# Kernel tuning notes

Hardware: AMD Instinct MI355X
Metric: run time of the kernel (lower is better)

The kernel has to match this reference:

```python
import jax, jax.numpy as jnp
import numpy as np

B, S, D = 2, 2048, 1024
N_HEADS = 16
HEAD_DIM = D // N_HEADS  # 64, even for RoPE
THETA = 10000.0


def rope_tables(seq, head_dim, dtype=jnp.float32):
    half = head_dim // 2
    freqs = 1.0 / (THETA ** (jnp.arange(half, dtype=jnp.float32) / half))
    angles = jnp.arange(seq, dtype=jnp.float32)[:, None] * freqs[None, :]  # [S, half]
    return jnp.cos(angles).astype(dtype), jnp.sin(angles).astype(dtype)


def apply_rope_interleaved(x, cos, sin):
    # x: [b, h, s, d]; even/odd interleaving
    x_even = x[..., 0::2]
    x_odd = x[..., 1::2]
    r_even = x_even * cos - x_odd * sin
    r_odd = x_even * sin + x_odd * cos
    # interleave back: stack on last axis then reshape
    out = jnp.stack([r_even, r_odd], axis=-1).reshape(x.shape)
    return out


def setup_inputs() -> dict:
    key = jax.random.key(0)
    ks = jax.random.split(key, 6)
    scale = 1.0 / np.sqrt(D)
    return {
        "x": jax.random.normal(ks[0], (B, S, D), dtype=jnp.float32),
        "Wq": jax.random.normal(ks[1], (D, D), dtype=jnp.float32) * scale,
        "Wk": jax.random.normal(ks[2], (D, D), dtype=jnp.float32) * scale,
        "Wv": jax.random.normal(ks[3], (D, D), dtype=jnp.float32) * scale,
        "Wo": jax.random.normal(ks[4], (D, D), dtype=jnp.float32) * scale,
        "bo": jnp.zeros((D,), dtype=jnp.float32),
    }


def reference(x, Wq, Wk, Wv, Wo, bo):
    b, s, _ = x.shape
    # QKV projections (no bias), split heads -> [b, h, s, hd]
    def proj(W):
        return jnp.einsum('bsd,de->bse', x, W).reshape(b, s, N_HEADS, HEAD_DIM).transpose(0, 2, 1, 3)
    q, k, v = proj(Wq), proj(Wk), proj(Wv)

    cos, sin = rope_tables(s, HEAD_DIM, x.dtype)  # [s, hd//2]
    q = apply_rope_interleaved(q, cos, sin)
    k = apply_rope_interleaved(k, cos, sin)

    scale = 1.0 / jnp.sqrt(jnp.asarray(HEAD_DIM, dtype=x.dtype))
    scores = jnp.einsum('bhqd,bhkd->bhqk', q, k) * scale  # [b, h, s, s]
    causal = jnp.tril(jnp.ones((s, s), dtype=bool))
    scores = jnp.where(causal[None, None], scores, jnp.asarray(-jnp.inf, dtype=scores.dtype))
    attn = jax.nn.softmax(scores, axis=-1)
    ctx = jnp.einsum('bhqk,bhkd->bhqd', attn, v)  # [b, h, s, hd]
    ctx = ctx.transpose(0, 2, 1, 3).reshape(b, s, N_HEADS * HEAD_DIM)
    return jnp.einsum('bsd,de->bse', ctx, Wo) + bo
```

## Files before the change

### kernel.cpp

```cpp
#include <hip/hip_runtime.h>
#include <hip/hip_bf16.h>
#include <math.h>

constexpr int Bb   = 2;
constexpr int S    = 2048;
constexpr int D    = 1024;
constexpr int H    = 16;
constexpr int Dh   = 64;
constexpr int HALF = 32;
constexpr int M    = Bb * S;
constexpr int K    = 1024;
constexpr int N    = 1024;

typedef __attribute__((ext_vector_type(8))) short short8;
typedef __attribute__((ext_vector_type(4))) float f32x4;

__device__ __forceinline__ unsigned short f2bf(float f) {
    unsigned int u = __float_as_uint(f);
    unsigned int r = (u + 0x7fffu + ((u >> 16) & 1u)) >> 16;
    return (unsigned short)r;
}

__device__ __forceinline__ void gl_lds16(const unsigned short* g, unsigned short* lds_base) {
    __builtin_amdgcn_global_load_lds(
        (const __attribute__((address_space(1))) unsigned int*)g,
        (__attribute__((address_space(3))) unsigned int*)lds_base, 16, 0, 0);
}

__global__ __launch_bounds__(256) void prep_kernel(
    const float* __restrict__ x,
    const float* W0, const float* W1, const float* W2, const float* W3,
    unsigned short* __restrict__ xb,
    unsigned short* T0, unsigned short* T1, unsigned short* T2, unsigned short* T3,
    float* __restrict__ cosT, float* __restrict__ sinT)
{
    __shared__ float tile[64][65];
    const int bid = blockIdx.x;
    const int tid = threadIdx.x;

    if (bid < 256) {
        int idx = bid * 256 + tid;
        int s = idx >> 5;
        int i = idx & 31;
        double freq = exp(-(double)i * (log(10000.0) / 32.0));
        double ang  = (double)s * freq;
        cosT[idx] = (float)cos(ang);
        sinT[idx] = (float)sin(ang);
    } else if (bid < 256 + 4096) {
        size_t i = (size_t)(bid - 256) * 256 + tid;
        float4 v = *(const float4*)(x + i * 4);
        ushort4 pk;
        pk.x = f2bf(v.x); pk.y = f2bf(v.y); pk.z = f2bf(v.z); pk.w = f2bf(v.w);
        *(ushort4*)(xb + i * 4) = pk;
    } else {
        int wb = bid - 4352;
        int z  = wb >> 8;
        int rem = wb & 255;
        const float* W = (z == 0) ? W0 : (z == 1) ? W1 : (z == 2) ? W2 : W3;
        unsigned short* T = (z == 0) ? T0 : (z == 1) ? T1 : (z == 2) ? T2 : T3;
        const int bk = (rem >> 4) * 64;
        const int bn = (rem & 15) * 64;
        const int lr = tid >> 4;
        const int lc = (tid & 15) * 4;

        #pragma unroll
        for (int i = 0; i < 4; ++i) {
            int r = lr + i * 16;
            float4 v = *(const float4*)(W + (size_t)(bk + r) * N + bn + lc);
            tile[r][lc + 0] = v.x; tile[r][lc + 1] = v.y;
            tile[r][lc + 2] = v.z; tile[r][lc + 3] = v.w;
        }
        __syncthreads();
        #pragma unroll
        for (int i = 0; i < 4; ++i) {
            int nr = lr + i * 16;
            ushort4 pk;
            pk.x = f2bf(tile[lc + 0][nr]);
            pk.y = f2bf(tile[lc + 1][nr]);
            pk.z = f2bf(tile[lc + 2][nr]);
            pk.w = f2bf(tile[lc + 3][nr]);
            *(ushort4*)(T + (size_t)(bn + nr) * K + bk + lc) = pk;
        }
    }
}

__global__ __launch_bounds__(256) void gemm_qkv_kernel(
    const unsigned short* __restrict__ A,
    const unsigned short* __restrict__ BT,
    unsigned short* outQ, unsigned short* outK, unsigned short* outV,
    const float* __restrict__ cosT, const float* __restrict__ sinT)
{
    constexpr int AST = 128 * 32;
    constexpr int BST = 128 * 32;
    __shared__ __align__(16) unsigned short As[2 * AST];
    __shared__ __align__(16) unsigned short Bs[2 * BST];

    const int tid  = threadIdx.x;
    const int wave = tid >> 6;
    const int lane = tid & 63;
    const int col  = lane & 15;
    const int quad = lane >> 4;
    const int wy   = wave >> 1;
    const int wx   = wave & 1;

    const int mbase = blockIdx.y * 128;
    const int nbase = blockIdx.x * 128;

    const int srow   = lane >> 2;
    const int schunk = lane & 3;

    const unsigned short* pA0;
    const unsigned short* pA1;
    {
        int tr0 = wave * 16 + srow;
        int tr1 = 64 + wave * 16 + srow;
        pA0 = A + (size_t)(mbase + tr0) * K + ((schunk + (tr0 >> 1)) & 3) * 8;
        pA1 = A + (size_t)(mbase + tr1) * K + ((schunk + (tr1 >> 1)) & 3) * 8;
    }
    const unsigned short* pB0;
    const unsigned short* pB1;
    {
        int tr0 = wave * 16 + srow;
        int tr1 = 64 + wave * 16 + srow;
        pB0 = BT + (size_t)(nbase + tr0) * K + ((schunk + (tr0 >> 1)) & 3) * 8;
        pB1 = BT + (size_t)(nbase + tr1) * K + ((schunk + (tr1 >> 1)) & 3) * 8;
    }
    unsigned short* dA0 = &As[(wave * 16) * 32];
    unsigned short* dA1 = &As[(64 + wave * 16) * 32];
    unsigned short* dB0 = &Bs[(wave * 16) * 32];
    unsigned short* dB1 = &Bs[(64 + wave * 16) * 32];

    int aoff[4], boff[4];
    #pragma unroll
    for (int mi = 0; mi < 4; ++mi) {
        int r = wy * 64 + mi * 16 + col;
        aoff[mi] = r * 32 + ((quad - (r >> 1)) & 3) * 8;
    }
    #pragma unroll
    for (int ni = 0; ni < 4; ++ni) {
        int r = wx * 64 + ni * 16 + col;
        boff[ni] = r * 32 + ((quad - (r >> 1)) & 3) * 8;
    }

    f32x4 acc[4][4];
    #pragma unroll
    for (int mi = 0; mi < 4; ++mi)
        #pragma unroll
        for (int ni = 0; ni < 4; ++ni) acc[mi][ni] = (f32x4)0.f;

    auto stage = [&](int buf) {
        gl_lds16(pA0, dA0 + buf * AST);  pA0 += 32;
        gl_lds16(pA1, dA1 + buf * AST);  pA1 += 32;
        gl_lds16(pB0, dB0 + buf * BST);  pB0 += 32;
        gl_lds16(pB1, dB1 + buf * BST);  pB1 += 32;
    };
    auto compute = [&](int buf) {
        const unsigned short* Ac = &As[buf * AST];
        const unsigned short* Bc = &Bs[buf * BST];
        short8 af[4], bfr[4];
        #pragma unroll
        for (int mi = 0; mi < 4; ++mi) af[mi] = *(const short8*)&Ac[aoff[mi]];
        #pragma unroll
        for (int ni = 0; ni < 4; ++ni) bfr[ni] = *(const short8*)&Bc[boff[ni]];
        #pragma unroll
        for (int mi = 0; mi < 4; ++mi)
            #pragma unroll
            for (int ni = 0; ni < 4; ++ni)
                acc[mi][ni] = __builtin_amdgcn_mfma_f32_16x16x32_bf16(af[mi], bfr[ni], acc[mi][ni], 0, 0, 0);
    };

    stage(0);
    #pragma unroll 1
    for (int kk = 0; kk < 32; kk += 2) {
        __syncthreads();
        if (kk + 1 < 32) stage(1);
        compute(0);
        __syncthreads();
        if (kk + 2 < 32) stage(0);
        compute(1);
    }

    const int z = nbase >> 10;
    if (z < 2) {
        unsigned short* o = z ? outK : outQ;
        #pragma unroll
        for (int ni = 0; ni < 4; ++ni) {
            int nl = (nbase & 1023) + wx * 64 + ni * 16 + col;
            int h = nl >> 6, dh0 = nl & 63, p = dh0 >> 1;
            bool even = !(dh0 & 1);
            #pragma unroll
            for (int mi = 0; mi < 4; ++mi)
                #pragma unroll
                for (int reg = 0; reg < 4; ++reg) {
                    int m_g = mbase + wy * 64 + mi * 16 + quad * 4 + reg;
                    int b = m_g >> 11, s = m_g & 2047;
                    float v = acc[mi][ni][reg];
                    float part = __shfl_xor(v, 1, 64);
                    float c = cosT[s * HALF + p], sn = sinT[s * HALF + p];
                    float r = even ? (v * c - part * sn) : (v * c + part * sn);
                    o[((size_t)(b * H + h) * S + s) * Dh + dh0] = f2bf(r);
                }
        }
    } else {
        unsigned short* o = outV;
        #pragma unroll
        for (int ni = 0; ni < 4; ++ni) {
            int nl = (nbase & 1023) + wx * 64 + ni * 16 + col;
            int h = nl >> 6, dh0 = nl & 63;
            #pragma unroll
            for (int mi = 0; mi < 4; ++mi) {
                int m0g = mbase + wy * 64 + mi * 16 + quad * 4;
                int b = m0g >> 11, s = m0g & 2047;
                ushort4 pk;
                pk.x = f2bf(acc[mi][ni][0]);
                pk.y = f2bf(acc[mi][ni][1]);
                pk.z = f2bf(acc[mi][ni][2]);
                pk.w = f2bf(acc[mi][ni][3]);
                *(ushort4*)&o[((size_t)(b * H + h) * Dh + dh0) * S + s] = pk;
            }
        }
    }
}

__global__ __launch_bounds__(256) void gemm_out_kernel(
    const unsigned short* __restrict__ A,
    const unsigned short* __restrict__ BT,
    float* __restrict__ outO, const float* __restrict__ bias)
{
    constexpr int BK   = 64;
    constexpr int ABUF = 128 * BK;
    constexpr int BBUF = 64 * BK;
    __shared__ __align__(16) unsigned short As[2 * ABUF];
    __shared__ __align__(16) unsigned short Bs[2 * BBUF];

    const int tid  = threadIdx.x;
    const int wave = tid >> 6;
    const int lane = tid & 63;
    const int col  = lane & 15;
    const int quad = lane >> 4;
    const int wy   = wave >> 1;
    const int wx   = wave & 1;

    const int mbase = blockIdx.y * 128;
    const int nbase = blockIdx.x * 64;

    const int srow8 = lane >> 3;
    const int sch8  = lane & 7;

    const unsigned short* pA[4];
    unsigned short* dA[4];
    #pragma unroll
    for (int w = 0; w < 4; ++w) {
        int base = wave * 32 + w * 8;
        int tr = base + srow8;
        pA[w] = A + (size_t)(mbase + tr) * K + ((sch8 + (tr >> 1)) & 7) * 8;
        dA[w] = &As[base * BK];
    }
    const unsigned short* pB[2];
    unsigned short* dB[2];
    #pragma unroll
    for (int w = 0; w < 2; ++w) {
        int base = wave * 16 + w * 8;
        int tr = base + srow8;
        pB[w] = BT + (size_t)(nbase + tr) * K + ((sch8 + (tr >> 1)) & 7) * 8;
        dB[w] = &Bs[base * BK];
    }

    int aoff[2][4], boff[2][2];
    #pragma unroll
    for (int ks = 0; ks < 2; ++ks) {
        #pragma unroll
        for (int mi = 0; mi < 4; ++mi) {
            int r = wy * 64 + mi * 16 + col;
            aoff[ks][mi] = r * BK + (((ks * 4 + quad) - (r >> 1)) & 7) * 8;
        }
        #pragma unroll
        for (int ni = 0; ni < 2; ++ni) {
            int r = wx * 32 + ni * 16 + col;
            boff[ks][ni] = r * BK + (((ks * 4 + quad) - (r >> 1)) & 7) * 8;
        }
    }

    f32x4 acc[4][2];
    #pragma unroll
    for (int mi = 0; mi < 4; ++mi)
        #pragma unroll
        for (int ni = 0; ni < 2; ++ni) acc[mi][ni] = (f32x4)0.f;

    auto stage = [&](int buf) {
        #pragma unroll
        for (int w = 0; w < 4; ++w) { gl_lds16(pA[w], dA[w] + buf * ABUF); pA[w] += BK; }
        #pragma unroll
        for (int w = 0; w < 2; ++w) { gl_lds16(pB[w], dB[w] + buf * BBUF); pB[w] += BK; }
    };
    auto compute = [&](int buf) {
        const unsigned short* Ac = &As[buf * ABUF];
        const unsigned short* Bc = &Bs[buf * BBUF];
        #pragma unroll
        for (int ks = 0; ks < 2; ++ks) {
            short8 af[4], bfr[2];
            #pragma unroll
            for (int mi = 0; mi < 4; ++mi) af[mi] = *(const short8*)&Ac[aoff[ks][mi]];
            #pragma unroll
            for (int ni = 0; ni < 2; ++ni) bfr[ni] = *(const short8*)&Bc[boff[ks][ni]];
            #pragma unroll
            for (int mi = 0; mi < 4; ++mi)
                #pragma unroll
                for (int ni = 0; ni < 2; ++ni)
                    acc[mi][ni] = __builtin_amdgcn_mfma_f32_16x16x32_bf16(af[mi], bfr[ni], acc[mi][ni], 0, 0, 0);
        }
    };

    stage(0);
    #pragma unroll 1
    for (int kk = 0; kk < 16; kk += 2) {
        __syncthreads();
        if (kk + 1 < 16) stage(1);
        compute(0);
        __syncthreads();
        if (kk + 2 < 16) stage(0);
        compute(1);
    }

    #pragma unroll
    for (int ni = 0; ni < 2; ++ni) {
        int n_g = nbase + wx * 32 + ni * 16 + col;
        float bv = bias[n_g];
        #pragma unroll
        for (int mi = 0; mi < 4; ++mi)
            #pragma unroll
            for (int reg = 0; reg < 4; ++reg) {
                int m_g = mbase + wy * 64 + mi * 16 + quad * 4 + reg;
                outO[(size_t)m_g * N + n_g] = acc[mi][ni][reg] + bv;
            }
    }
}

__global__ __launch_bounds__(256) void attn_mfma_kernel(
    const unsigned short* __restrict__ q, const unsigned short* __restrict__ k,
    const unsigned short* __restrict__ vt, unsigned short* __restrict__ ctx)
{
    constexpr int TSZ = 64 * 64;
    __shared__ __align__(16) unsigned short Ks[4 * TSZ];
    __shared__ __align__(16) unsigned short Vs[4 * TSZ];
    __shared__ __align__(16) unsigned short Ps[4][16 * 72];

    const int tid  = threadIdx.x;
    const int wave = tid >> 6;
    const int lane = tid & 63;
    const int col  = lane & 15;
    const int quad = lane >> 4;
    const int l8   = lane >> 3, cp = lane & 7;

    const int bh = blockIdx.y;
    const unsigned short* qb = q  + (size_t)bh * S * Dh;
    const unsigned short* kb = k  + (size_t)bh * S * Dh;
    const unsigned short* vb = vt + (size_t)bh * Dh * S;
    const int b = bh >> 4, h = bh & 15;

    unsigned short* dk0 = &Ks[(wave * 16 + 0) * 64];
    unsigned short* dk1 = &Ks[(wave * 16 + 8) * 64];
    unsigned short* dv0 = &Vs[(wave * 16 + 0) * 64];
    unsigned short* dv1 = &Vs[(wave * 16 + 8) * 64];

    int foff[2][4];
    #pragma unroll
    for (int ks = 0; ks < 2; ++ks)
        #pragma unroll
        for (int nt = 0; nt < 4; ++nt) {
            int r = nt * 16 + col;
            foff[ks][nt] = r * 64 + (((ks * 4 + quad) - r) & 7) * 8;
        }
    int poffW[4][4];
    #pragma unroll
    for (int nt = 0; nt < 4; ++nt)
        #pragma unroll
        for (int reg = 0; reg < 4; ++reg)
            poffW[nt][reg] = (quad * 4 + reg) * 72 + nt * 16 + col;
    const int poffR0 = col * 72 + quad * 8;

    for (int phase = 0; phase < 2; ++phase) {
        const int qt  = phase ? (31 - (int)blockIdx.x) : (int)blockIdx.x;
        const int wr0 = qt * 64 + wave * 16;

        const unsigned short *pk0, *pk1, *pv0, *pv1, *ok0, *ok1, *ov0, *ov1;
        {
            int r0 = wave * 16 + l8, r1 = r0 + 8;
            pk0 = kb + (size_t)r0 * Dh + ((cp + r0) & 7) * 8;
            pk1 = kb + (size_t)r1 * Dh + ((cp + r1) & 7) * 8;
            pv0 = vb + (size_t)r0 * S + ((cp + r0) & 7) * 8;
            pv1 = vb + (size_t)r1 * S + ((cp + r1) & 7) * 8;
            ok0 = pk0 + 64 * Dh; ok1 = pk1 + 64 * Dh;
            ov0 = pv0 + 64;      ov1 = pv1 + 64;
        }

        __syncthreads();
        gl_lds16(pk0, dk0); gl_lds16(pk1, dk1);
        gl_lds16(pv0, dv0); gl_lds16(pv1, dv1);
        if (qt >= 1) {
            gl_lds16(ok0, dk0 + TSZ); gl_lds16(ok1, dk1 + TSZ);
            gl_lds16(ov0, dv0 + TSZ); gl_lds16(ov1, dv1 + TSZ);
        }
        pk0 += 128 * Dh; pk1 += 128 * Dh; pv0 += 128; pv1 += 128;
        ok0 += 128 * Dh; ok1 += 128 * Dh; ov0 += 128; ov1 += 128;

        short8 qfrag[2];
        #pragma unroll
        for (int ks = 0; ks < 2; ++ks)
            qfrag[ks] = *(const short8*)(qb + (size_t)(wr0 + col) * Dh + ks * 32 + quad * 8);

        f32x4 O[4];
        float lacc[4];
        #pragma unroll
        for (int nt = 0; nt < 4; ++nt) O[nt] = (f32x4)0.f;
        #pragma unroll
        for (int r = 0; r < 4; ++r) lacc[r] = 0.f;

        auto subtile = [&](const unsigned short* Kc, const unsigned short* Vc, int t) {
            f32x4 sacc[4];
            #pragma unroll
            for (int nt = 0; nt < 4; ++nt) sacc[nt] = (f32x4)0.f;
            #pragma unroll
            for (int ks = 0; ks < 2; ++ks)
                #pragma unroll
                for (int nt = 0; nt < 4; ++nt) {
                    short8 kf = *(const short8*)&Kc[foff[ks][nt]];
                    sacc[nt] = __builtin_amdgcn_mfma_f32_16x16x32_bf16(qfrag[ks], kf, sacc[nt], 0, 0, 0);
                }
            float pb[4][4];
            #pragma unroll
            for (int nt = 0; nt < 4; ++nt) {
                int key_l = nt * 16 + col;
                #pragma unroll
                for (int reg = 0; reg < 4; ++reg) {
                    float e = __expf(fmaf(sacc[nt][reg], 0.125f, -8.0f));
                    if (t == qt && key_l > wave * 16 + quad * 4 + reg) e = 0.f;
                    pb[nt][reg] = e;
                }
            }
            #pragma unroll
            for (int reg = 0; reg < 4; ++reg)
                lacc[reg] += (pb[0][reg] + pb[1][reg]) + (pb[2][reg] + pb[3][reg]);
            #pragma unroll
            for (int nt = 0; nt < 4; ++nt)
                #pragma unroll
                for (int reg = 0; reg < 4; ++reg)
                    Ps[wave][poffW[nt][reg]] = f2bf(pb[nt][reg]);
            #pragma unroll
            for (int ks = 0; ks < 2; ++ks) {
                short8 pf = *(const short8*)&Ps[wave][poffR0 + ks * 32];
                #pragma unroll
                for (int nt = 0; nt < 4; ++nt) {
                    short8 vf = *(const short8*)&Vc[foff[ks][nt]];
                    O[nt] = __builtin_amdgcn_mfma_f32_16x16x32_bf16(pf, vf, O[nt], 0, 0, 0);
                }
            }
        };

        const int nint = (qt >> 1) + 1;
        for (int i = 0; i < nint; ++i) {
            __syncthreads();
            const int ta = 2 * i;
            if (ta + 2 <= qt) {
                const int nb = ((i + 1) & 1) * 2 * TSZ;
                gl_lds16(pk0, dk0 + nb); gl_lds16(pk1, dk1 + nb);
                gl_lds16(pv0, dv0 + nb); gl_lds16(pv1, dv1 + nb);
                if (ta + 3 <= qt) {
                    gl_lds16(ok0, dk0 + nb + TSZ); gl_lds16(ok1, dk1 + nb + TSZ);
                    gl_lds16(ov0, dv0 + nb + TSZ); gl_lds16(ov1, dv1 + nb + TSZ);
                }
                pk0 += 128 * Dh; pk1 += 128 * Dh; pv0 += 128; pv1 += 128;
                ok0 += 128 * Dh; ok1 += 128 * Dh; ov0 += 128; ov1 += 128;
            }
            const unsigned short* Kc = &Ks[(i & 1) * 2 * TSZ];
            const unsigned short* Vc = &Vs[(i & 1) * 2 * TSZ];
            subtile(Kc, Vc, ta);
            if (ta + 1 <= qt) subtile(Kc + TSZ, Vc + TSZ, ta + 1);
        }

        #pragma unroll
        for (int reg = 0; reg < 4; ++reg) {
            float s = lacc[reg];
            #pragma unroll
            for (int off = 1; off <= 8; off <<= 1)
                s += __shfl_xor(s, off, 64);
            lacc[reg] = s;
        }

        #pragma unroll
        for (int reg = 0; reg < 4; ++reg) {
            float inv = 1.0f / lacc[reg];
            int rg = wr0 + quad * 4 + reg;
            unsigned short* dst = ctx + ((size_t)b * S + rg) * 1024 + h * 64 + col;
            #pragma unroll
            for (int nt = 0; nt < 4; ++nt)
                dst[nt * 16] = f2bf(O[nt][reg] * inv);
        }
    }
}

extern "C" void kernel_launch(void* const* d_in, const int* in_sizes, int n_in,
                              void* d_out, int out_size, void* d_ws, size_t ws_size,
                              hipStream_t stream) {
    const float* x  = (const float*)d_in[0];
    const float* Wq = (const float*)d_in[1];
    const float* Wk = (const float*)d_in[2];
    const float* Wv = (const float*)d_in[3];
    const float* Wo = (const float*)d_in[4];
    const float* bo = (const float*)d_in[5];
    float* out = (float*)d_out;

    const size_t MK  = (size_t)M * K;
    const size_t NK  = (size_t)N * K;
    const size_t QKV = (size_t)Bb * H * S * Dh;

    unsigned short* xb   = (unsigned short*)d_ws;
    unsigned short* WqT  = xb  + MK;
    unsigned short* WkT  = WqT + NK;
    unsigned short* WvT  = WkT + NK;
    unsigned short* WoT  = WvT + NK;
    unsigned short* qbuf = WoT + NK;
    unsigned short* kbuf = qbuf + QKV;
    unsigned short* vtb  = kbuf + QKV;
    unsigned short* ctxb = vtb  + QKV;
    float* cosT = (float*)(ctxb + QKV);
    float* sinT = cosT + (size_t)S * HALF;

    prep_kernel<<<5376, 256, 0, stream>>>(x, Wq, Wk, Wv, Wo,
                                          xb, WqT, WkT, WvT, WoT, cosT, sinT);

    gemm_qkv_kernel<<<dim3(24, 32), 256, 0, stream>>>(
        xb, WqT, qbuf, kbuf, vtb, cosT, sinT);

    attn_mfma_kernel<<<dim3(16, Bb * H), 256, 0, stream>>>(qbuf, kbuf, vtb, ctxb);

    gemm_out_kernel<<<dim3(16, 32), 256, 0, stream>>>(ctxb, WoT, out, bo);
}
```

Measured before the change: 200.6 us.

## Share K/V tile loads across paired query tiles in attention; shrink out-GEMM tile

The attention kernel now processes both of its paired query tiles (small and large) in a single pass over the key/value sequence. Each K/V tile is loaded into LDS once and reused by both query tiles, where before there were two separate sequential passes. This halves K/V traffic and barrier count per block, at the cost of more registers for the duplicated accumulators. Separately, the output GEMM tile is reduced from 128x64 to 64x64 and the grid doubled, which gives more blocks for occupancy on the many CUs.

```diff
diff --git a/kernel.cpp b/kernel.cpp
--- a/kernel.cpp
+++ b/kernel.cpp
@@ -228,7 +228,7 @@
     float* __restrict__ outO, const float* __restrict__ bias)
 {
     constexpr int BK   = 64;
-    constexpr int ABUF = 128 * BK;
+    constexpr int ABUF = 64 * BK;
     constexpr int BBUF = 64 * BK;
     __shared__ __align__(16) unsigned short As[2 * ABUF];
     __shared__ __align__(16) unsigned short Bs[2 * BBUF];
@@ -241,37 +241,30 @@
     const int wy   = wave >> 1;
     const int wx   = wave & 1;
 
-    const int mbase = blockIdx.y * 128;
+    const int mbase = blockIdx.y * 64;
     const int nbase = blockIdx.x * 64;
 
     const int srow8 = lane >> 3;
     const int sch8  = lane & 7;
 
-    const unsigned short* pA[4];
-    unsigned short* dA[4];
-    #pragma unroll
-    for (int w = 0; w < 4; ++w) {
-        int base = wave * 32 + w * 8;
-        int tr = base + srow8;
-        pA[w] = A + (size_t)(mbase + tr) * K + ((sch8 + (tr >> 1)) & 7) * 8;
-        dA[w] = &As[base * BK];
-    }
-    const unsigned short* pB[2];
-    unsigned short* dB[2];
+    const unsigned short *pA[2], *pB[2];
+    unsigned short *dA[2], *dB[2];
     #pragma unroll
     for (int w = 0; w < 2; ++w) {
         int base = wave * 16 + w * 8;
         int tr = base + srow8;
+        pA[w] = A  + (size_t)(mbase + tr) * K + ((sch8 + (tr >> 1)) & 7) * 8;
         pB[w] = BT + (size_t)(nbase + tr) * K + ((sch8 + (tr >> 1)) & 7) * 8;
+        dA[w] = &As[base * BK];
         dB[w] = &Bs[base * BK];
     }
 
-    int aoff[2][4], boff[2][2];
+    int aoff[2][2], boff[2][2];
     #pragma unroll
     for (int ks = 0; ks < 2; ++ks) {
         #pragma unroll
-        for (int mi = 0; mi < 4; ++mi) {
-            int r = wy * 64 + mi * 16 + col;
+        for (int mi = 0; mi < 2; ++mi) {
+            int r = wy * 32 + mi * 16 + col;
             aoff[ks][mi] = r * BK + (((ks * 4 + quad) - (r >> 1)) & 7) * 8;
         }
         #pragma unroll
@@ -281,15 +274,15 @@
         }
     }
 
-    f32x4 acc[4][2];
-    #pragma unroll
-    for (int mi = 0; mi < 4; ++mi)
+    f32x4 acc[2][2];
+    #pragma unroll
+    for (int mi = 0; mi < 2; ++mi)
         #pragma unroll
         for (int ni = 0; ni < 2; ++ni) acc[mi][ni] = (f32x4)0.f;
 
     auto stage = [&](int buf) {
         #pragma unroll
-        for (int w = 0; w < 4; ++w) { gl_lds16(pA[w], dA[w] + buf * ABUF); pA[w] += BK; }
+        for (int w = 0; w < 2; ++w) { gl_lds16(pA[w], dA[w] + buf * ABUF); pA[w] += BK; }
         #pragma unroll
         for (int w = 0; w < 2; ++w) { gl_lds16(pB[w], dB[w] + buf * BBUF); pB[w] += BK; }
     };
@@ -298,13 +291,13 @@
         const unsigned short* Bc = &Bs[buf * BBUF];
         #pragma unroll
         for (int ks = 0; ks < 2; ++ks) {
-            short8 af[4], bfr[2];
-            #pragma unroll
-            for (int mi = 0; mi < 4; ++mi) af[mi] = *(const short8*)&Ac[aoff[ks][mi]];
+            short8 af[2], bfr[2];
+            #pragma unroll
+            for (int mi = 0; mi < 2; ++mi) af[mi] = *(const short8*)&Ac[aoff[ks][mi]];
             #pragma unroll
             for (int ni = 0; ni < 2; ++ni) bfr[ni] = *(const short8*)&Bc[boff[ks][ni]];
             #pragma unroll
-            for (int mi = 0; mi < 4; ++mi)
+            for (int mi = 0; mi < 2; ++mi)
                 #pragma unroll
                 for (int ni = 0; ni < 2; ++ni)
                     acc[mi][ni] = __builtin_amdgcn_mfma_f32_16x16x32_bf16(af[mi], bfr[ni], acc[mi][ni], 0, 0, 0);
@@ -327,10 +320,10 @@
         int n_g = nbase + wx * 32 + ni * 16 + col;
         float bv = bias[n_g];
         #pragma unroll
-        for (int mi = 0; mi < 4; ++mi)
+        for (int mi = 0; mi < 2; ++mi)
             #pragma unroll
             for (int reg = 0; reg < 4; ++reg) {
-                int m_g = mbase + wy * 64 + mi * 16 + quad * 4 + reg;
+                int m_g = mbase + wy * 32 + mi * 16 + quad * 4 + reg;
                 outO[(size_t)m_g * N + n_g] = acc[mi][ni][reg] + bv;
             }
     }
@@ -352,7 +345,10 @@
     const int quad = lane >> 4;
     const int l8   = lane >> 3, cp = lane & 7;
 
-    const int bh = blockIdx.y;
+    const int bh  = blockIdx.y;
+    const int x   = blockIdx.x;
+    const int qtb = 31 - x;
+    const int qts = x;
     const unsigned short* qb = q  + (size_t)bh * S * Dh;
     const unsigned short* kb = k  + (size_t)bh * S * Dh;
     const unsigned short* vb = vt + (size_t)bh * Dh * S;
@@ -379,68 +375,71 @@
             poffW[nt][reg] = (quad * 4 + reg) * 72 + nt * 16 + col;
     const int poffR0 = col * 72 + quad * 8;
 
-    for (int phase = 0; phase < 2; ++phase) {
-        const int qt  = phase ? (31 - (int)blockIdx.x) : (int)blockIdx.x;
-        const int wr0 = qt * 64 + wave * 16;
-
-        const unsigned short *pk0, *pk1, *pv0, *pv1, *ok0, *ok1, *ov0, *ov1;
-        {
-            int r0 = wave * 16 + l8, r1 = r0 + 8;
-            pk0 = kb + (size_t)r0 * Dh + ((cp + r0) & 7) * 8;
-            pk1 = kb + (size_t)r1 * Dh + ((cp + r1) & 7) * 8;
-            pv0 = vb + (size_t)r0 * S + ((cp + r0) & 7) * 8;
-            pv1 = vb + (size_t)r1 * S + ((cp + r1) & 7) * 8;
-            ok0 = pk0 + 64 * Dh; ok1 = pk1 + 64 * Dh;
-            ov0 = pv0 + 64;      ov1 = pv1 + 64;
-        }
-
-        __syncthreads();
-        gl_lds16(pk0, dk0); gl_lds16(pk1, dk1);
-        gl_lds16(pv0, dv0); gl_lds16(pv1, dv1);
-        if (qt >= 1) {
-            gl_lds16(ok0, dk0 + TSZ); gl_lds16(ok1, dk1 + TSZ);
-            gl_lds16(ov0, dv0 + TSZ); gl_lds16(ov1, dv1 + TSZ);
-        }
-        pk0 += 128 * Dh; pk1 += 128 * Dh; pv0 += 128; pv1 += 128;
-        ok0 += 128 * Dh; ok1 += 128 * Dh; ov0 += 128; ov1 += 128;
-
-        short8 qfrag[2];
+    const unsigned short *pk0, *pk1, *pv0, *pv1, *ok0, *ok1, *ov0, *ov1;
+    {
+        int r0 = wave * 16 + l8, r1 = r0 + 8;
+        pk0 = kb + (size_t)r0 * Dh + ((cp + r0) & 7) * 8;
+        pk1 = kb + (size_t)r1 * Dh + ((cp + r1) & 7) * 8;
+        pv0 = vb + (size_t)r0 * S + ((cp + r0) & 7) * 8;
+        pv1 = vb + (size_t)r1 * S + ((cp + r1) & 7) * 8;
+        ok0 = pk0 + 64 * Dh; ok1 = pk1 + 64 * Dh;
+        ov0 = pv0 + 64;      ov1 = pv1 + 64;
+    }
+
+    gl_lds16(pk0, dk0); gl_lds16(pk1, dk1);
+    gl_lds16(pv0, dv0); gl_lds16(pv1, dv1);
+    gl_lds16(ok0, dk0 + TSZ); gl_lds16(ok1, dk1 + TSZ);
+    gl_lds16(ov0, dv0 + TSZ); gl_lds16(ov1, dv1 + TSZ);
+    pk0 += 128 * Dh; pk1 += 128 * Dh; pv0 += 128; pv1 += 128;
+    ok0 += 128 * Dh; ok1 += 128 * Dh; ov0 += 128; ov1 += 128;
+
+    short8 qfrag[2][2];
+    f32x4 O[2][4];
+    float lacc[2][4];
+    int wr0[2];
+    #pragma unroll
+    for (int qi = 0; qi < 2; ++qi) {
+        wr0[qi] = (qi ? qts : qtb) * 64 + wave * 16;
         #pragma unroll
         for (int ks = 0; ks < 2; ++ks)
-            qfrag[ks] = *(const short8*)(qb + (size_t)(wr0 + col) * Dh + ks * 32 + quad * 8);
-
-        f32x4 O[4];
-        float lacc[4];
-        #pragma unroll
-        for (int nt = 0; nt < 4; ++nt) O[nt] = (f32x4)0.f;
-        #pragma unroll
-        for (int r = 0; r < 4; ++r) lacc[r] = 0.f;
-
-        auto subtile = [&](const unsigned short* Kc, const unsigned short* Vc, int t) {
-            f32x4 sacc[4];
-            #pragma unroll
-            for (int nt = 0; nt < 4; ++nt) sacc[nt] = (f32x4)0.f;
-            #pragma unroll
-            for (int ks = 0; ks < 2; ++ks)
-                #pragma unroll
-                for (int nt = 0; nt < 4; ++nt) {
-                    short8 kf = *(const short8*)&Kc[foff[ks][nt]];
-                    sacc[nt] = __builtin_amdgcn_mfma_f32_16x16x32_bf16(qfrag[ks], kf, sacc[nt], 0, 0, 0);
-                }
+            qfrag[qi][ks] = *(const short8*)(qb + (size_t)(wr0[qi] + col) * Dh + ks * 32 + quad * 8);
+        #pragma unroll
+        for (int nt = 0; nt < 4; ++nt) O[qi][nt] = (f32x4)0.f;
+        #pragma unroll
+        for (int r = 0; r < 4; ++r) lacc[qi][r] = 0.f;
+    }
+
+    auto subtile = [&](const unsigned short* Kc, const unsigned short* Vc,
+                       int t, bool both) {
+        f32x4 sacc[2][4];
+        #pragma unroll
+        for (int nt = 0; nt < 4; ++nt) { sacc[0][nt] = (f32x4)0.f; sacc[1][nt] = (f32x4)0.f; }
+        #pragma unroll
+        for (int ks = 0; ks < 2; ++ks)
+            #pragma unroll
+            for (int nt = 0; nt < 4; ++nt) {
+                short8 kf = *(const short8*)&Kc[foff[ks][nt]];
+                sacc[0][nt] = __builtin_amdgcn_mfma_f32_16x16x32_bf16(qfrag[0][ks], kf, sacc[0][nt], 0, 0, 0);
+                if (both)
+                    sacc[1][nt] = __builtin_amdgcn_mfma_f32_16x16x32_bf16(qfrag[1][ks], kf, sacc[1][nt], 0, 0, 0);
+            }
+        const int nqi = both ? 2 : 1;
+        for (int qi = 0; qi < nqi; ++qi) {
+            const int qt_i = qi ? qts : qtb;
             float pb[4][4];
             #pragma unroll
             for (int nt = 0; nt < 4; ++nt) {
                 int key_l = nt * 16 + col;
                 #pragma unroll
                 for (int reg = 0; reg < 4; ++reg) {
-                    float e = __expf(fmaf(sacc[nt][reg], 0.125f, -8.0f));
-                    if (t == qt && key_l > wave * 16 + quad * 4 + reg) e = 0.f;
+                    float e = __expf(fmaf(sacc[qi][nt][reg], 0.125f, -8.0f));
+                    if (t == qt_i && key_l > wave * 16 + quad * 4 + reg) e = 0.f;
                     pb[nt][reg] = e;
                 }
             }
             #pragma unroll
             for (int reg = 0; reg < 4; ++reg)
-                lacc[reg] += (pb[0][reg] + pb[1][reg]) + (pb[2][reg] + pb[3][reg]);
+                lacc[qi][reg] += (pb[0][reg] + pb[1][reg]) + (pb[2][reg] + pb[3][reg]);
             #pragma unroll
             for (int nt = 0; nt < 4; ++nt)
                 #pragma unroll
@@ -452,49 +451,48 @@
                 #pragma unroll
                 for (int nt = 0; nt < 4; ++nt) {
                     short8 vf = *(const short8*)&Vc[foff[ks][nt]];
-                    O[nt] = __builtin_amdgcn_mfma_f32_16x16x32_bf16(pf, vf, O[nt], 0, 0, 0);
+                    O[qi][nt] = __builtin_amdgcn_mfma_f32_16x16x32_bf16(pf, vf, O[qi][nt], 0, 0, 0);
                 }
             }
-        };
-
-        const int nint = (qt >> 1) + 1;
-        for (int i = 0; i < nint; ++i) {
-            __syncthreads();
-            const int ta = 2 * i;
-            if (ta + 2 <= qt) {
-                const int nb = ((i + 1) & 1) * 2 * TSZ;
-                gl_lds16(pk0, dk0 + nb); gl_lds16(pk1, dk1 + nb);
-                gl_lds16(pv0, dv0 + nb); gl_lds16(pv1, dv1 + nb);
-                if (ta + 3 <= qt) {
-                    gl_lds16(ok0, dk0 + nb + TSZ); gl_lds16(ok1, dk1 + nb + TSZ);
-                    gl_lds16(ov0, dv0 + nb + TSZ); gl_lds16(ov1, dv1 + nb + TSZ);
-                }
-                pk0 += 128 * Dh; pk1 += 128 * Dh; pv0 += 128; pv1 += 128;
-                ok0 += 128 * Dh; ok1 += 128 * Dh; ov0 += 128; ov1 += 128;
+        }
+    };
+
+    const int nint = (qtb + 2) >> 1;
+    for (int i = 0; i < nint; ++i) {
+        __syncthreads();
+        const int ta = 2 * i;
+        if (ta + 2 <= qtb) {
+            const int nb = ((i + 1) & 1) * 2 * TSZ;
+            gl_lds16(pk0, dk0 + nb); gl_lds16(pk1, dk1 + nb);
+            gl_lds16(pv0, dv0 + nb); gl_lds16(pv1, dv1 + nb);
+            if (ta + 3 <= qtb) {
+                gl_lds16(ok0, dk0 + nb + TSZ); gl_lds16(ok1, dk1 + nb + TSZ);
+                gl_lds16(ov0, dv0 + nb + TSZ); gl_lds16(ov1, dv1 + nb + TSZ);
             }
-            const unsigned short* Kc = &Ks[(i & 1) * 2 * TSZ];
-            const unsigned short* Vc = &Vs[(i & 1) * 2 * TSZ];
-            subtile(Kc, Vc, ta);
-            if (ta + 1 <= qt) subtile(Kc + TSZ, Vc + TSZ, ta + 1);
-        }
-
+            pk0 += 128 * Dh; pk1 += 128 * Dh; pv0 += 128; pv1 += 128;
+            ok0 += 128 * Dh; ok1 += 128 * Dh; ov0 += 128; ov1 += 128;
+        }
+        const unsigned short* Kc = &Ks[(i & 1) * 2 * TSZ];
+        const unsigned short* Vc = &Vs[(i & 1) * 2 * TSZ];
+        subtile(Kc, Vc, ta, ta <= qts);
+        if (ta + 1 <= qtb)
+            subtile(Kc + TSZ, Vc + TSZ, ta + 1, ta + 1 <= qts);
+    }
+
+    #pragma unroll
+    for (int qi = 0; qi < 2; ++qi) {
         #pragma unroll
         for (int reg = 0; reg < 4; ++reg) {
-            float s = lacc[reg];
+            float s = lacc[qi][reg];
             #pragma unroll
             for (int off = 1; off <= 8; off <<= 1)
                 s += __shfl_xor(s, off, 64);
-            lacc[reg] = s;
-        }
-
-        #pragma unroll
-        for (int reg = 0; reg < 4; ++reg) {
-            float inv = 1.0f / lacc[reg];
-            int rg = wr0 + quad * 4 + reg;
+            float inv = 1.0f / s;
+            int rg = wr0[qi] + quad * 4 + reg;
             unsigned short* dst = ctx + ((size_t)b * S + rg) * 1024 + h * 64 + col;
             #pragma unroll
             for (int nt = 0; nt < 4; ++nt)
-                dst[nt * 16] = f2bf(O[nt][reg] * inv);
+                dst[nt * 16] = f2bf(O[qi][nt][reg] * inv);
         }
     }
 }
@@ -534,5 +532,5 @@
 
     attn_mfma_kernel<<<dim3(16, Bb * H), 256, 0, stream>>>(qbuf, kbuf, vtb, ctxb);
 
-    gemm_out_kernel<<<dim3(16, 32), 256, 0, stream>>>(ctxb, WoT, out, bo);
-}
+    gemm_out_kernel<<<dim3(16, 64), 256, 0, stream>>>(ctxb, WoT, out, bo);
+}
```

New measurement: 206.2 us. 2.8% more time.
